# Kernel tuning notes

Measured on AMD Instinct MI355X. Metric: run time of the kernel, lower is better.

## Reference

```python
import jax, jax.numpy as jnp
import numpy as np

B, D, H = 8192, 1024, 4096


def setup_inputs() -> dict:
    key = jax.random.key(0)
    ks = jax.random.split(key, 8)
    s_in = 1.0 / np.sqrt(D)
    s_hid = 1.0 / np.sqrt(H)
    return {
        "x": jax.random.normal(ks[0], (B, D), dtype=jnp.float32),
        "Wr": jax.random.normal(ks[1], (D, 1), dtype=jnp.float32) * s_in,
        "br": jnp.zeros((1,), dtype=jnp.float32),
        "W1l": jax.random.normal(ks[2], (D, H), dtype=jnp.float32) * s_in,
        "b1l": jnp.zeros((H,), dtype=jnp.float32),
        "W2l": jax.random.normal(ks[3], (H, D), dtype=jnp.float32) * s_hid,
        "b2l": jnp.zeros((D,), dtype=jnp.float32),
        "W1r": jax.random.normal(ks[4], (D, H), dtype=jnp.float32) * s_in,
        "b1r": jnp.zeros((H,), dtype=jnp.float32),
        "W2r": jax.random.normal(ks[5], (H, D), dtype=jnp.float32) * s_hid,
        "b2r": jnp.zeros((D,), dtype=jnp.float32),
    }


def _expert(x, W1, b1, W2, b2):
    # 2-layer MLP expert: [B, D] -> [B, H] -> [B, D]
    h = jax.nn.relu(x @ W1 + b1)
    return h @ W2 + b2


def reference(x, Wr, br, W1l, b1l, W2l, b2l, W1r, b1r, W2r, b2r):
    # Router probability p in (0, 1): [B, 1]
    p = jax.nn.sigmoid(x @ Wr + br)
    left = _expert(x, W1l, b1l, W2l, b2l)   # [B, D]
    right = _expert(x, W1r, b1r, W2r, b2r)  # [B, D]
    # soft_decision branch: convex combination of children per sample
    return p * left + (1.0 - p) * right
```

## Files before the change

### kernel.cpp

```cpp
#include <hip/hip_runtime.h>
#include <hip/hip_bf16.h>
#include <cstdint>
#include <cstddef>

#define B_DIM  8192
#define D_DIM  1024
#define H_DIM  4096
#define H2_DIM 8192

using bf16 = __hip_bfloat16;
typedef __attribute__((ext_vector_type(8))) short bf16x8;
typedef __attribute__((ext_vector_type(4))) float f32x4;

__global__ __launch_bounds__(256) void cast_f32_to_bf16(const float* __restrict__ in,
                                                        bf16* __restrict__ out, int n_vec8) {
    int i = blockIdx.x * 256 + threadIdx.x;
    if (i >= n_vec8) return;
    const float4* src = reinterpret_cast<const float4*>(in) + (size_t)i * 2;
    float4 a = src[0], b = src[1];
    union { bf16 h[8]; int4 u; } r;
    r.h[0] = __float2bfloat16(a.x); r.h[1] = __float2bfloat16(a.y);
    r.h[2] = __float2bfloat16(a.z); r.h[3] = __float2bfloat16(a.w);
    r.h[4] = __float2bfloat16(b.x); r.h[5] = __float2bfloat16(b.y);
    r.h[6] = __float2bfloat16(b.z); r.h[7] = __float2bfloat16(b.w);
    reinterpret_cast<int4*>(out)[i] = r.u;
}

__global__ __launch_bounds__(256) void router_kernel(const float* __restrict__ x,
                                                     const float* __restrict__ Wr,
                                                     const float* __restrict__ br,
                                                     float* __restrict__ p) {
    int wave = threadIdx.x >> 6, lane = threadIdx.x & 63;
    int row = blockIdx.x * 4 + wave;
    const float* xr = x + (size_t)row * D_DIM;
    float sum = 0.f;
#pragma unroll
    for (int it = 0; it < 4; ++it) {
        int k = it * 256 + lane * 4;
        float4 xv = *reinterpret_cast<const float4*>(xr + k);
        float4 wv = *reinterpret_cast<const float4*>(Wr + k);
        sum += xv.x * wv.x + xv.y * wv.y + xv.z * wv.z + xv.w * wv.w;
    }
#pragma unroll
    for (int off = 32; off >= 1; off >>= 1) sum += __shfl_down(sum, off, 64);
    if (lane == 0) p[row] = 1.f / (1.f + expf(-(sum + br[0])));
}

__global__ __launch_bounds__(256) void transpose_cast_kernel(const float* __restrict__ src,
                                                             int R, int C,
                                                             bf16* __restrict__ dst, int dstLD) {
    __shared__ float tile[32][33];
    int c0 = blockIdx.x * 32, r0 = blockIdx.y * 32;
    int tx = threadIdx.x & 31, ty = threadIdx.x >> 5;
#pragma unroll
    for (int i = 0; i < 32; i += 8)
        tile[ty + i][tx] = src[(size_t)(r0 + ty + i) * C + c0 + tx];
    __syncthreads();
#pragma unroll
    for (int i = 0; i < 32; i += 8)
        dst[(size_t)(c0 + ty + i) * dstLD + r0 + tx] = __float2bfloat16(tile[tx][ty + i]);
}

template<int NBH, int EPI>
__global__ __launch_bounds__(512, 2) void gemm8(const bf16* __restrict__ A,
                                                const bf16* __restrict__ Bt,
                                                void* __restrict__ Cout,
                                                int N, int K, int NT, int nbx,
                                                const float* __restrict__ p,
                                                const float* __restrict__ bias_l,
                                                const float* __restrict__ bias_r) {
    constexpr int NREP  = 2 * NBH;
    constexpr int MPP   = (NBH == 2) ? 2 : 4;
    constexpr int HALF  = 16384;
    constexpr int NHALF = 2 + NBH;
    constexpr int BUFB  = NHALF * HALF;
    __shared__ __align__(16) char lds[2 * BUFB];

    const int tid  = threadIdx.x;
    const int wid  = tid >> 6, lane = tid & 63;
    const int wr   = wid >> 2, wcn = wid & 3;

    const int cpx     = (int)gridDim.x >> 3;
    const int logical = ((int)blockIdx.x & 7) * cpx + ((int)blockIdx.x >> 3);
    const int by = logical / nbx, bx = logical - by * nbx;
    const int bm = by * 256, bn = bx * (NBH * 128);

    const int      r0   = tid >> 3;
    const uint32_t cswz = (uint32_t)(((tid & 7) ^ (r0 & 7)) << 3);
    uint32_t offA[2], offB[NBH];
#pragma unroll
    for (int h = 0; h < 2; ++h)    offA[h] = (uint32_t)(bm + h * 128 + r0) * (uint32_t)K + cswz;
#pragma unroll
    for (int h = 0; h < NBH; ++h)  offB[h] = (uint32_t)(bn + h * 128 + r0) * (uint32_t)K + cswz;

#define STGH(G, P, HI, EOFF) do {                                                             \
    _Pragma("unroll") for (int j_ = 0; j_ < 2; ++j_)                                          \
        __builtin_amdgcn_global_load_lds(                                                     \
            (const __attribute__((address_space(1))) uint32_t*)((G) + (size_t)(EOFF) + (size_t)(j_ * 64) * (size_t)K), \
            (__attribute__((address_space(3))) uint32_t*)(lds + (P) * BUFB + (HI) * HALF + j_ * 8192 + wid * 1024), \
            16, 0, 0);                                                                        \
} while (0)

    const int      lrow = lane & 15, kg8 = lane >> 4;
    const uint32_t swz  = (uint32_t)((kg8 ^ (lrow & 7)) << 4);
    const uint32_t sAb  = (uint32_t)(wr * HALF) + (uint32_t)(lrow * 128) + swz;
    const int      colt0 = wcn * (NREP * 16);
    const uint32_t sBb  = (uint32_t)((2 + (colt0 >> 7)) * HALF) + (uint32_t)(((colt0 & 127) + lrow) * 128) + swz;

#define RD(o) (*reinterpret_cast<const bf16x8*>(lds + (o)))

    bf16x8 bf[NREP][2];
    bf16x8 af[MPP][2];
    f32x4 acc[8][NREP];
#pragma unroll
    for (int m = 0; m < 8; ++m)
#pragma unroll
        for (int n = 0; n < NREP; ++n) acc[m][n] = (f32x4){0.f, 0.f, 0.f, 0.f};

#define RDBF(P) do {                                                                          \
    _Pragma("unroll") for (int n_ = 0; n_ < NREP; ++n_)                                       \
      _Pragma("unroll") for (int k_ = 0; k_ < 2; ++k_)                                        \
        bf[n_][k_] = RD((uint32_t)((P) * BUFB) + ((sBb + (uint32_t)(n_ * 2048)) ^ (uint32_t)(k_ << 6))); \
} while (0)

#define RDAF(P, M0) do {                                                                      \
    _Pragma("unroll") for (int m_ = 0; m_ < MPP; ++m_)                                        \
      _Pragma("unroll") for (int k_ = 0; k_ < 2; ++k_)                                        \
        af[m_][k_] = RD((uint32_t)((P) * BUFB) + ((sAb + (uint32_t)((((M0) + m_) * 2048))) ^ (uint32_t)(k_ << 6))); \
} while (0)

#define MFMAQ(M0) do {                                                                        \
    _Pragma("unroll") for (int m_ = 0; m_ < MPP; ++m_)                                        \
      _Pragma("unroll") for (int n_ = 0; n_ < NREP; ++n_)                                     \
        _Pragma("unroll") for (int k_ = 0; k_ < 2; ++k_)                                      \
          acc[(M0) + m_][n_] = __builtin_amdgcn_mfma_f32_16x16x32_bf16(af[m_][k_], bf[n_][k_], acc[(M0) + m_][n_], 0, 0, 0); \
} while (0)

#define VMC(NSTR) do { asm volatile("s_waitcnt vmcnt(" NSTR ")" ::: "memory");                \
                       __builtin_amdgcn_sched_barrier(0); } while (0)

#define PH(P, M0, FIRSTP, STAGES, WAITS, TRAILB) do {                                         \
    if (FIRSTP) RDBF(P);                                                                      \
    RDAF(P, M0);                                                                              \
    STAGES                                                                                    \
    __builtin_amdgcn_s_barrier();                                                             \
    asm volatile("s_waitcnt lgkmcnt(0)" ::: "memory");                                        \
    __builtin_amdgcn_sched_barrier(0);                                                        \
    __builtin_amdgcn_s_setprio(1);                                                            \
    MFMAQ(M0);                                                                                \
    __builtin_amdgcn_s_setprio(0);                                                            \
    __builtin_amdgcn_sched_barrier(0);                                                        \
    WAITS                                                                                     \
    if (TRAILB) { __builtin_amdgcn_s_barrier(); __builtin_amdgcn_sched_barrier(0); }          \
} while (0)

    if constexpr (NBH == 2) {
        STGH(A, 0, 0, offA[0]); STGH(A, 0, 1, offA[1]);
        STGH(Bt, 0, 2, offB[0]); STGH(Bt, 0, 3, offB[1]);
        STGH(Bt, 1, 2, offB[0] + 64); STGH(Bt, 1, 3, offB[1] + 64);
        VMC("4");
    } else {
        STGH(A, 0, 0, offA[0]); STGH(A, 0, 1, offA[1]); STGH(Bt, 0, 2, offB[0]);
        STGH(Bt, 1, 2, offB[0] + 64);
        VMC("2");
    }
    __builtin_amdgcn_s_barrier();
    __builtin_amdgcn_sched_barrier(0);

    const int NIT = NT >> 1;
    for (int i = 0; i < NIT - 1; ++i) {
        const uint32_t k1 = (uint32_t)(2 * i + 1) * 64u;
        const uint32_t k2 = (uint32_t)(2 * i + 2) * 64u;
        const uint32_t k3 = (uint32_t)(2 * i + 3) * 64u;
        if constexpr (NBH == 2) {
            PH(0, 0, true,  { STGH(A, 1, 0, offA[0] + k1); }, , true);
            PH(0, 2, false, { STGH(A, 1, 1, offA[1] + k1); }, , true);
            PH(0, 4, false, { STGH(Bt, 0, 2, offB[0] + k2); }, , true);
            PH(0, 6, false, { STGH(Bt, 0, 3, offB[1] + k2); }, VMC("4");, true);
            PH(1, 0, true,  { STGH(A, 0, 0, offA[0] + k2); }, , true);
            PH(1, 2, false, { STGH(A, 0, 1, offA[1] + k2); }, , true);
            PH(1, 4, false, { STGH(Bt, 1, 2, offB[0] + k3); }, , true);
            PH(1, 6, false, { STGH(Bt, 1, 3, offB[1] + k3); }, VMC("4");, true);
        } else {
            PH(0, 0, true,  { STGH(A, 1, 0, offA[0] + k1); STGH(A, 1, 1, offA[1] + k1); }, , true);
            PH(0, 4, false, { STGH(Bt, 0, 2, offB[0] + k2); }, VMC("2");, true);
            PH(1, 0, true,  { STGH(A, 0, 0, offA[0] + k2); STGH(A, 0, 1, offA[1] + k2); }, , true);
            PH(1, 4, false, { STGH(Bt, 1, 2, offB[0] + k3); }, VMC("2");, true);
        }
    }
    {
        const uint32_t kl = (uint32_t)(NT - 1) * 64u;
        if constexpr (NBH == 2) {
            PH(0, 0, true,  { STGH(A, 1, 0, offA[0] + kl); }, , true);
            PH(0, 2, false, { STGH(A, 1, 1, offA[1] + kl); }, , true);
            PH(0, 4, false, , , true);
            PH(0, 6, false, , VMC("0");, true);
            PH(1, 0, true,  , , true);
            PH(1, 2, false, , , true);
            PH(1, 4, false, , , true);
            PH(1, 6, false, , , false);
        } else {
            PH(0, 0, true,  { STGH(A, 1, 0, offA[0] + kl); STGH(A, 1, 1, offA[1] + kl); }, , true);
            PH(0, 4, false, , VMC("0");, true);
            PH(1, 0, true,  , , true);
            PH(1, 4, false, , , false);
        }
    }

    const int crow0 = bm + wr * 128 + (kg8 << 2);
    const int ccol0 = bn + colt0 + lrow;

    if (EPI == 1) {
        bf16* __restrict__ Ho = (bf16*)Cout;
#pragma unroll
        for (int n = 0; n < NREP; ++n) {
            const int col = ccol0 + n * 16;
            const bool left = col < H_DIM;
            const float bias = left ? bias_l[col] : bias_r[col - H_DIM];
#pragma unroll
            for (int m = 0; m < 8; ++m) {
#pragma unroll
                for (int j = 0; j < 4; ++j) {
                    const int row = crow0 + m * 16 + j;
                    const float pw = p[row];
                    const float scale = left ? pw : 1.f - pw;
                    const float v = fmaxf(acc[m][n][j] + bias, 0.f) * scale;
                    Ho[(size_t)row * N + col] = __float2bfloat16(v);
                }
            }
        }
    } else {
        float* __restrict__ Co = (float*)Cout;
#pragma unroll
        for (int n = 0; n < NREP; ++n) {
            const int col = ccol0 + n * 16;
            const float bl = bias_l[col];
            const float brr = bias_r[col];
#pragma unroll
            for (int m = 0; m < 8; ++m) {
#pragma unroll
                for (int j = 0; j < 4; ++j) {
                    const int row = crow0 + m * 16 + j;
                    const float pw = p[row];
                    Co[(size_t)row * N + col] = acc[m][n][j] + pw * bl + (1.f - pw) * brr;
                }
            }
        }
    }
#undef PH
#undef VMC
#undef MFMAQ
#undef RDAF
#undef RDBF
#undef RD
#undef STGH
}

extern "C" void kernel_launch(void* const* d_in, const int* in_sizes, int n_in,
                              void* d_out, int out_size, void* d_ws, size_t ws_size,
                              hipStream_t stream) {
    const float* x   = (const float*)d_in[0];
    const float* Wr  = (const float*)d_in[1];
    const float* br  = (const float*)d_in[2];
    const float* W1l = (const float*)d_in[3];
    const float* b1l = (const float*)d_in[4];
    const float* W2l = (const float*)d_in[5];
    const float* b2l = (const float*)d_in[6];
    const float* W1r = (const float*)d_in[7];
    const float* b1r = (const float*)d_in[8];
    const float* W2r = (const float*)d_in[9];
    const float* b2r = (const float*)d_in[10];
    float* out = (float*)d_out;

    char* ws = (char*)d_ws;
    bf16*  x_bf = (bf16*)(ws);
    bf16*  W1t  = (bf16*)(ws + (size_t)(16u << 20));
    bf16*  hbuf = (bf16*)(ws + (size_t)(32u << 20));
    float* pbuf = (float*)(ws + (size_t)(160u << 20));
    bf16*  W2t  = x_bf;

    cast_f32_to_bf16<<<(B_DIM * D_DIM / 8 + 255) / 256, 256, 0, stream>>>(x, x_bf, B_DIM * D_DIM / 8);
    router_kernel<<<B_DIM / 4, 256, 0, stream>>>(x, Wr, br, pbuf);

    transpose_cast_kernel<<<dim3(H_DIM / 32, D_DIM / 32), 256, 0, stream>>>(W1l, D_DIM, H_DIM, W1t, D_DIM);
    transpose_cast_kernel<<<dim3(H_DIM / 32, D_DIM / 32), 256, 0, stream>>>(W1r, D_DIM, H_DIM,
                                                                            W1t + (size_t)H_DIM * D_DIM, D_DIM);
    gemm8<2, 1><<<1024, 512, 0, stream>>>(x_bf, W1t, hbuf, H2_DIM, D_DIM, D_DIM / 64, 32,
                                          pbuf, b1l, b1r);

    transpose_cast_kernel<<<dim3(D_DIM / 32, H_DIM / 32), 256, 0, stream>>>(W2l, H_DIM, D_DIM, W2t, H2_DIM);
    transpose_cast_kernel<<<dim3(D_DIM / 32, H_DIM / 32), 256, 0, stream>>>(W2r, H_DIM, D_DIM, W2t + H_DIM, H2_DIM);

    gemm8<1, 0><<<256, 512, 0, stream>>>(hbuf, W2t, out, D_DIM, H2_DIM, H2_DIM / 64, 8,
                                         pbuf, b2l, b2r);
}
```

Measured before the change: 461.9 us.

## Reorder GEMM phases into 2x2 quadrants, stage epilogue through LDS, merge transposes

```diff
diff --git a/kernel.cpp b/kernel.cpp
--- a/kernel.cpp
+++ b/kernel.cpp
@@ -46,19 +46,29 @@
     if (lane == 0) p[row] = 1.f / (1.f + expf(-(sum + br[0])));
 }
 
-__global__ __launch_bounds__(256) void transpose_cast_kernel(const float* __restrict__ src,
-                                                             int R, int C,
-                                                             bf16* __restrict__ dst, int dstLD) {
-    __shared__ float tile[32][33];
-    int c0 = blockIdx.x * 32, r0 = blockIdx.y * 32;
-    int tx = threadIdx.x & 31, ty = threadIdx.x >> 5;
-#pragma unroll
-    for (int i = 0; i < 32; i += 8)
-        tile[ty + i][tx] = src[(size_t)(r0 + ty + i) * C + c0 + tx];
+__global__ __launch_bounds__(256) void transpose_cast2(const float* __restrict__ srcA,
+                                                       const float* __restrict__ srcB,
+                                                       int C,
+                                                       bf16* __restrict__ dstA,
+                                                       bf16* __restrict__ dstB, int dstLD) {
+    __shared__ float tile[64][65];
+    const float* src = blockIdx.z ? srcB : srcA;
+    bf16*       dst = blockIdx.z ? dstB : dstA;
+    const int c0 = blockIdx.x * 64, r0 = blockIdx.y * 64;
+    const int tx = threadIdx.x & 63, ty = threadIdx.x >> 6;
+#pragma unroll
+    for (int k = 0; k < 16; ++k)
+        tile[k * 4 + ty][tx] = src[(size_t)(r0 + k * 4 + ty) * C + c0 + tx];
     __syncthreads();
 #pragma unroll
-    for (int i = 0; i < 32; i += 8)
-        dst[(size_t)(c0 + ty + i) * dstLD + r0 + tx] = __float2bfloat16(tile[tx][ty + i]);
+    for (int k = 0; k < 8; ++k) {
+        const int gr = k * 8 + (threadIdx.x >> 5);
+        const int rc = (threadIdx.x & 31) * 2;
+        union { bf16 h[2]; uint32_t u; } w;
+        w.h[0] = __float2bfloat16(tile[rc][gr]);
+        w.h[1] = __float2bfloat16(tile[rc + 1][gr]);
+        *reinterpret_cast<uint32_t*>(&dst[(size_t)(c0 + gr) * dstLD + r0 + rc]) = w.u;
+    }
 }
 
 template<int NBH, int EPI>
@@ -70,11 +80,13 @@
                                                 const float* __restrict__ bias_l,
                                                 const float* __restrict__ bias_r) {
     constexpr int NREP  = 2 * NBH;
-    constexpr int MPP   = (NBH == 2) ? 2 : 4;
     constexpr int HALF  = 16384;
     constexpr int NHALF = 2 + NBH;
     constexpr int BUFB  = NHALF * HALF;
-    __shared__ __align__(16) char lds[2 * BUFB];
+    constexpr int EP_PITCH = 264;
+    constexpr size_t LDSB = (EPI == 1 && (size_t)256 * EP_PITCH * 2 > (size_t)2 * BUFB)
+                              ? (size_t)256 * EP_PITCH * 2 : (size_t)2 * BUFB;
+    __shared__ __align__(16) char lds[LDSB];
 
     const int tid  = threadIdx.x;
     const int wid  = tid >> 6, lane = tid & 63;
@@ -109,128 +121,148 @@
 
 #define RD(o) (*reinterpret_cast<const bf16x8*>(lds + (o)))
 
-    bf16x8 bf[NREP][2];
-    bf16x8 af[MPP][2];
+    bf16x8 bf[2][2];
+    bf16x8 af[4][2];
     f32x4 acc[8][NREP];
 #pragma unroll
     for (int m = 0; m < 8; ++m)
 #pragma unroll
         for (int n = 0; n < NREP; ++n) acc[m][n] = (f32x4){0.f, 0.f, 0.f, 0.f};
 
-#define RDBF(P) do {                                                                          \
-    _Pragma("unroll") for (int n_ = 0; n_ < NREP; ++n_)                                       \
+#define RDA(P, MH) do {                                                                       \
+    _Pragma("unroll") for (int m_ = 0; m_ < 4; ++m_)                                          \
       _Pragma("unroll") for (int k_ = 0; k_ < 2; ++k_)                                        \
-        bf[n_][k_] = RD((uint32_t)((P) * BUFB) + ((sBb + (uint32_t)(n_ * 2048)) ^ (uint32_t)(k_ << 6))); \
-} while (0)
-
-#define RDAF(P, M0) do {                                                                      \
-    _Pragma("unroll") for (int m_ = 0; m_ < MPP; ++m_)                                        \
+        af[m_][k_] = RD((uint32_t)((P) * BUFB) + ((sAb + (uint32_t)((((MH) * 4 + m_) * 2048))) ^ (uint32_t)(k_ << 6))); \
+} while (0)
+
+#define RDB(P, NH) do {                                                                       \
+    _Pragma("unroll") for (int n_ = 0; n_ < 2; ++n_)                                          \
       _Pragma("unroll") for (int k_ = 0; k_ < 2; ++k_)                                        \
-        af[m_][k_] = RD((uint32_t)((P) * BUFB) + ((sAb + (uint32_t)((((M0) + m_) * 2048))) ^ (uint32_t)(k_ << 6))); \
-} while (0)
-
-#define MFMAQ(M0) do {                                                                        \
-    _Pragma("unroll") for (int m_ = 0; m_ < MPP; ++m_)                                        \
-      _Pragma("unroll") for (int n_ = 0; n_ < NREP; ++n_)                                     \
+        bf[n_][k_] = RD((uint32_t)((P) * BUFB) + ((sBb + (uint32_t)((((NH) * 2 + n_) * 2048))) ^ (uint32_t)(k_ << 6))); \
+} while (0)
+
+#define MFMAQ(MH, NH) do {                                                                    \
+    _Pragma("unroll") for (int m_ = 0; m_ < 4; ++m_)                                          \
+      _Pragma("unroll") for (int n_ = 0; n_ < 2; ++n_)                                        \
         _Pragma("unroll") for (int k_ = 0; k_ < 2; ++k_)                                      \
-          acc[(M0) + m_][n_] = __builtin_amdgcn_mfma_f32_16x16x32_bf16(af[m_][k_], bf[n_][k_], acc[(M0) + m_][n_], 0, 0, 0); \
+          acc[(MH) * 4 + m_][(NH) * 2 + n_] =                                                 \
+            __builtin_amdgcn_mfma_f32_16x16x32_bf16(af[m_][k_], bf[n_][k_],                   \
+                                                    acc[(MH) * 4 + m_][(NH) * 2 + n_], 0, 0, 0); \
 } while (0)
 
 #define VMC(NSTR) do { asm volatile("s_waitcnt vmcnt(" NSTR ")" ::: "memory");                \
                        __builtin_amdgcn_sched_barrier(0); } while (0)
 
-#define PH(P, M0, FIRSTP, STAGES, WAITS, TRAILB) do {                                         \
-    if (FIRSTP) RDBF(P);                                                                      \
-    RDAF(P, M0);                                                                              \
-    STAGES                                                                                    \
+#define PH(RR, MH, NH, STG, WT, TB) do {                                                      \
+    RR                                                                                        \
+    STG                                                                                       \
     __builtin_amdgcn_s_barrier();                                                             \
     asm volatile("s_waitcnt lgkmcnt(0)" ::: "memory");                                        \
     __builtin_amdgcn_sched_barrier(0);                                                        \
     __builtin_amdgcn_s_setprio(1);                                                            \
-    MFMAQ(M0);                                                                                \
+    MFMAQ(MH, NH);                                                                            \
     __builtin_amdgcn_s_setprio(0);                                                            \
     __builtin_amdgcn_sched_barrier(0);                                                        \
-    WAITS                                                                                     \
-    if (TRAILB) { __builtin_amdgcn_s_barrier(); __builtin_amdgcn_sched_barrier(0); }          \
+    WT                                                                                        \
+    if (TB) { __builtin_amdgcn_s_barrier(); __builtin_amdgcn_sched_barrier(0); }              \
 } while (0)
 
     if constexpr (NBH == 2) {
         STGH(A, 0, 0, offA[0]); STGH(A, 0, 1, offA[1]);
         STGH(Bt, 0, 2, offB[0]); STGH(Bt, 0, 3, offB[1]);
-        STGH(Bt, 1, 2, offB[0] + 64); STGH(Bt, 1, 3, offB[1] + 64);
+        STGH(Bt, 1, 2, offB[0] + 64); STGH(A, 1, 1, offA[1] + 64);
         VMC("4");
+        __builtin_amdgcn_s_barrier();
+        __builtin_amdgcn_sched_barrier(0);
+
+        for (int i = 0; i < (NT - 2) / 2; ++i) {
+            const uint32_t k1 = (uint32_t)(2 * i + 1) * 64u;
+            const uint32_t k2 = (uint32_t)(2 * i + 2) * 64u;
+            const uint32_t k3 = (uint32_t)(2 * i + 3) * 64u;
+            PH({RDA(0,0); RDB(0,0);}, 0, 0, {STGH(A, 1, 0, offA[0] + k1);}, , true);
+            PH({RDA(0,1);},           1, 0, {STGH(Bt, 1, 3, offB[1] + k1);}, , true);
+            PH({RDB(0,1);},           1, 1, {STGH(Bt, 0, 2, offB[0] + k2);}, , true);
+            PH({RDA(0,0);},           0, 1, {STGH(A, 0, 1, offA[1] + k2);}, VMC("4");, true);
+            PH({RDA(1,0); RDB(1,0);}, 0, 0, {STGH(A, 0, 0, offA[0] + k2);}, , true);
+            PH({RDA(1,1);},           1, 0, {STGH(Bt, 0, 3, offB[1] + k2);}, , true);
+            PH({RDB(1,1);},           1, 1, {STGH(Bt, 1, 2, offB[0] + k3);}, , true);
+            PH({RDA(1,0);},           0, 1, {STGH(A, 1, 1, offA[1] + k3);}, VMC("4");, true);
+        }
+        {
+            const uint32_t kl = (uint32_t)(NT - 1) * 64u;
+            PH({RDA(0,0); RDB(0,0);}, 0, 0, {STGH(A, 1, 0, offA[0] + kl);}, , true);
+            PH({RDA(0,1);},           1, 0, {STGH(Bt, 1, 3, offB[1] + kl);}, , true);
+            PH({RDB(0,1);},           1, 1, , , true);
+            PH({RDA(0,0);},           0, 1, , VMC("0");, true);
+        }
+        PH({RDA(1,0); RDB(1,0);}, 0, 0, , , true);
+        PH({RDA(1,1);},           1, 0, , , true);
+        PH({RDB(1,1);},           1, 1, , , true);
+        PH({RDA(1,0);},           0, 1, , , false);
     } else {
         STGH(A, 0, 0, offA[0]); STGH(A, 0, 1, offA[1]); STGH(Bt, 0, 2, offB[0]);
-        STGH(Bt, 1, 2, offB[0] + 64);
+        STGH(A, 1, 0, offA[0] + 64);
         VMC("2");
+        __builtin_amdgcn_s_barrier();
+        __builtin_amdgcn_sched_barrier(0);
+
+        for (int i = 0; i < (NT - 2) / 2; ++i) {
+            const uint32_t k1 = (uint32_t)(2 * i + 1) * 64u;
+            const uint32_t k2 = (uint32_t)(2 * i + 2) * 64u;
+            const uint32_t k3 = (uint32_t)(2 * i + 3) * 64u;
+            PH({RDA(0,0); RDB(0,0);}, 0, 0, {STGH(Bt, 1, 2, offB[0] + k1); STGH(A, 1, 1, offA[1] + k1);}, , true);
+            PH({RDA(0,1);},           1, 0, {STGH(A, 0, 0, offA[0] + k2);}, VMC("2");, true);
+            PH({RDA(1,0); RDB(1,0);}, 0, 0, {STGH(Bt, 0, 2, offB[0] + k2); STGH(A, 0, 1, offA[1] + k2);}, , true);
+            PH({RDA(1,1);},           1, 0, {STGH(A, 1, 0, offA[0] + k3);}, VMC("2");, true);
+        }
+        {
+            const uint32_t kl = (uint32_t)(NT - 1) * 64u;
+            PH({RDA(0,0); RDB(0,0);}, 0, 0, {STGH(Bt, 1, 2, offB[0] + kl); STGH(A, 1, 1, offA[1] + kl);}, , true);
+            PH({RDA(0,1);},           1, 0, , VMC("0");, true);
+        }
+        PH({RDA(1,0); RDB(1,0);}, 0, 0, , , true);
+        PH({RDA(1,1);},           1, 0, , , false);
     }
-    __builtin_amdgcn_s_barrier();
-    __builtin_amdgcn_sched_barrier(0);
-
-    const int NIT = NT >> 1;
-    for (int i = 0; i < NIT - 1; ++i) {
-        const uint32_t k1 = (uint32_t)(2 * i + 1) * 64u;
-        const uint32_t k2 = (uint32_t)(2 * i + 2) * 64u;
-        const uint32_t k3 = (uint32_t)(2 * i + 3) * 64u;
-        if constexpr (NBH == 2) {
-            PH(0, 0, true,  { STGH(A, 1, 0, offA[0] + k1); }, , true);
-            PH(0, 2, false, { STGH(A, 1, 1, offA[1] + k1); }, , true);
-            PH(0, 4, false, { STGH(Bt, 0, 2, offB[0] + k2); }, , true);
-            PH(0, 6, false, { STGH(Bt, 0, 3, offB[1] + k2); }, VMC("4");, true);
-            PH(1, 0, true,  { STGH(A, 0, 0, offA[0] + k2); }, , true);
-            PH(1, 2, false, { STGH(A, 0, 1, offA[1] + k2); }, , true);
-            PH(1, 4, false, { STGH(Bt, 1, 2, offB[0] + k3); }, , true);
-            PH(1, 6, false, { STGH(Bt, 1, 3, offB[1] + k3); }, VMC("4");, true);
-        } else {
-            PH(0, 0, true,  { STGH(A, 1, 0, offA[0] + k1); STGH(A, 1, 1, offA[1] + k1); }, , true);
-            PH(0, 4, false, { STGH(Bt, 0, 2, offB[0] + k2); }, VMC("2");, true);
-            PH(1, 0, true,  { STGH(A, 0, 0, offA[0] + k2); STGH(A, 0, 1, offA[1] + k2); }, , true);
-            PH(1, 4, false, { STGH(Bt, 1, 2, offB[0] + k3); }, VMC("2");, true);
-        }
-    }
-    {
-        const uint32_t kl = (uint32_t)(NT - 1) * 64u;
-        if constexpr (NBH == 2) {
-            PH(0, 0, true,  { STGH(A, 1, 0, offA[0] + kl); }, , true);
-            PH(0, 2, false, { STGH(A, 1, 1, offA[1] + kl); }, , true);
-            PH(0, 4, false, , , true);
-            PH(0, 6, false, , VMC("0");, true);
-            PH(1, 0, true,  , , true);
-            PH(1, 2, false, , , true);
-            PH(1, 4, false, , , true);
-            PH(1, 6, false, , , false);
-        } else {
-            PH(0, 0, true,  { STGH(A, 1, 0, offA[0] + kl); STGH(A, 1, 1, offA[1] + kl); }, , true);
-            PH(0, 4, false, , VMC("0");, true);
-            PH(1, 0, true,  , , true);
-            PH(1, 4, false, , , false);
-        }
-    }
-
-    const int crow0 = bm + wr * 128 + (kg8 << 2);
-    const int ccol0 = bn + colt0 + lrow;
 
     if (EPI == 1) {
+        __builtin_amdgcn_s_barrier();
         bf16* __restrict__ Ho = (bf16*)Cout;
-#pragma unroll
-        for (int n = 0; n < NREP; ++n) {
-            const int col = ccol0 + n * 16;
-            const bool left = col < H_DIM;
-            const float bias = left ? bias_l[col] : bias_r[col - H_DIM];
-#pragma unroll
-            for (int m = 0; m < 8; ++m) {
-#pragma unroll
-                for (int j = 0; j < 4; ++j) {
-                    const int row = crow0 + m * 16 + j;
-                    const float pw = p[row];
-                    const float scale = left ? pw : 1.f - pw;
-                    const float v = fmaxf(acc[m][n][j] + bias, 0.f) * scale;
-                    Ho[(size_t)row * N + col] = __float2bfloat16(v);
+        bf16* elds = (bf16*)lds;
+        const int er0 = wr * 128 + (kg8 << 2);
+        float biasv[4];
+        bool  leftv[4];
+#pragma unroll
+        for (int n = 0; n < 4; ++n) {
+            const int col = bn + colt0 + n * 16 + lrow;
+            leftv[n] = col < H_DIM;
+            biasv[n] = leftv[n] ? bias_l[col] : bias_r[col - H_DIM];
+        }
+#pragma unroll
+        for (int m = 0; m < 8; ++m) {
+#pragma unroll
+            for (int j = 0; j < 4; ++j) {
+                const int rl = er0 + m * 16 + j;
+                const float pw = p[bm + rl];
+#pragma unroll
+                for (int n = 0; n < 4; ++n) {
+                    const float scale = leftv[n] ? pw : 1.f - pw;
+                    const float v = fmaxf(acc[m][n][j] + biasv[n], 0.f) * scale;
+                    elds[rl * EP_PITCH + colt0 + n * 16 + lrow] = __float2bfloat16(v);
                 }
             }
         }
+        __builtin_amdgcn_s_barrier();
+#pragma unroll
+        for (int r = 0; r < 16; ++r) {
+            const int rl = r * 16 + (tid >> 5);
+            const int cb = (tid & 31) * 8;
+            int4 v = *reinterpret_cast<const int4*>(&elds[rl * EP_PITCH + cb]);
+            *reinterpret_cast<int4*>(&Ho[(size_t)(bm + rl) * N + bn + cb]) = v;
+        }
     } else {
         float* __restrict__ Co = (float*)Cout;
+        const int crow0 = bm + wr * 128 + (kg8 << 2);
+        const int ccol0 = bn + colt0 + lrow;
 #pragma unroll
         for (int n = 0; n < NREP; ++n) {
             const int col = ccol0 + n * 16;
@@ -250,8 +282,8 @@
 #undef PH
 #undef VMC
 #undef MFMAQ
-#undef RDAF
-#undef RDBF
+#undef RDB
+#undef RDA
 #undef RD
 #undef STGH
 }
@@ -282,14 +314,14 @@
     cast_f32_to_bf16<<<(B_DIM * D_DIM / 8 + 255) / 256, 256, 0, stream>>>(x, x_bf, B_DIM * D_DIM / 8);
     router_kernel<<<B_DIM / 4, 256, 0, stream>>>(x, Wr, br, pbuf);
 
-    transpose_cast_kernel<<<dim3(H_DIM / 32, D_DIM / 32), 256, 0, stream>>>(W1l, D_DIM, H_DIM, W1t, D_DIM);
-    transpose_cast_kernel<<<dim3(H_DIM / 32, D_DIM / 32), 256, 0, stream>>>(W1r, D_DIM, H_DIM,
-                                                                            W1t + (size_t)H_DIM * D_DIM, D_DIM);
+    transpose_cast2<<<dim3(H_DIM / 64, D_DIM / 64, 2), 256, 0, stream>>>(
+        W1l, W1r, H_DIM, W1t, W1t + (size_t)H_DIM * D_DIM, D_DIM);
+
     gemm8<2, 1><<<1024, 512, 0, stream>>>(x_bf, W1t, hbuf, H2_DIM, D_DIM, D_DIM / 64, 32,
                                           pbuf, b1l, b1r);
 
-    transpose_cast_kernel<<<dim3(D_DIM / 32, H_DIM / 32), 256, 0, stream>>>(W2l, H_DIM, D_DIM, W2t, H2_DIM);
-    transpose_cast_kernel<<<dim3(D_DIM / 32, H_DIM / 32), 256, 0, stream>>>(W2r, H_DIM, D_DIM, W2t + H_DIM, H2_DIM);
+    transpose_cast2<<<dim3(D_DIM / 64, H_DIM / 64, 2), 256, 0, stream>>>(
+        W2l, W2r, D_DIM, W2t, W2t + H_DIM, H2_DIM);
 
     gemm8<1, 0><<<256, 512, 0, stream>>>(hbuf, W2t, out, D_DIM, H2_DIM, H2_DIM / 64, 8,
                                          pbuf, b2l, b2r);
```

After: 431.8 us. 1.07x faster.
